# Performance work log

Measured on AMD Instinct MI355X. Metric: run time of the kernel, lower is better.

The kernel has to match this reference:

```python
import jax, jax.numpy as jnp
import numpy as np

N_NODES = 50000


def gcn_conv(x, src, dst, W, b):
    # PyG GCNConv: h = x @ W; symmetric norm with added self-loops; out = A_hat h + b
    h = x @ W
    deg = jax.ops.segment_sum(jnp.ones_like(src, dtype=h.dtype), dst,
                              num_segments=N_NODES) + 1.0  # +1 self-loop
    dis = jax.lax.rsqrt(deg)  # deg >= 1, safe
    msg = h[src] * (dis[src] * dis[dst])[:, None]          # [E,H] gather + scale
    agg = jax.ops.segment_sum(msg, dst, num_segments=N_NODES)
    agg = agg + h * (dis * dis)[:, None]                   # self-loop contribution
    return agg + b


def link_pred(zs, e, Wp, bp):
    # zs: [L,N,H]; gather endpoints along node dim, per-edge cross-layer Gram matrix
    s = zs[:, e[0]]                                # [L,E,H]
    d = zs[:, e[1]]                                # [L,E,H]
    dot = jnp.einsum('leh,meh->elm', s, d)         # [E,L,L] per-edge bmm
    emb = dot.reshape(dot.shape[0], -1)            # [E,L*L]
    return emb @ Wp + bp                           # [E,1] logits (activation=False)


def reference(x, ei, pos, neg, W0, b0, Wh, bh, Wp, bp):
    src, dst = ei[0], ei[1]
    h = jax.nn.relu(gcn_conv(x, src, dst, W0, b0))
    embs = [h]
    for i in range(Wh.shape[0]):  # fixed small layer count
        h = jax.nn.relu(gcn_conv(h, src, dst, Wh[i], bh[i]))
        embs.append(h)
    zs = jnp.stack(embs, axis=0)                   # [L,N,H]
    pos_pred = link_pred(zs, pos, Wp, bp)
    neg_pred = link_pred(zs, neg, Wp, bp)
    logits = jnp.concatenate([pos_pred, neg_pred], axis=0)  # [2E,1]
    # faithful to source: targets all zero except row index == n_pos set to 1
    targets = jnp.zeros_like(logits).at[pos_pred.shape[0]].set(1.0)
    # BCEWithLogitsLoss (mean, numerically stable)
    loss = jnp.mean(jnp.clip(logits, 0.0) - logits * targets
                    + jnp.log1p(jnp.exp(-jnp.abs(logits))))
    return loss


def setup_inputs():
    key = jax.random.key(0)
    ks = jax.random.split(key, 10)
    N, E, EP, IN, H, L = 50000, 800000, 100000, 128, 64, 4
    x = jax.random.normal(ks[0], (N, IN), jnp.float32)
    ei = jax.random.randint(ks[1], (2, E), 0, N, dtype=jnp.int32)
    pos = jax.random.randint(ks[2], (2, EP), 0, N, dtype=jnp.int32)
    neg = jax.random.randint(ks[3], (2, EP), 0, N, dtype=jnp.int32)
    def u(k, shape, fan_in):
        s = 1.0 / np.sqrt(fan_in)
        return jax.random.uniform(k, shape, jnp.float32, -s, s)
    W0 = u(ks[4], (IN, H), IN)
    b0 = u(ks[5], (H,), IN)
    Wh = u(ks[6], (L - 1, H, H), H)
    bh = u(ks[7], (L - 1, H), H)
    Wp = u(ks[8], (L * L, 1), L * L)
    bp = u(ks[9], (1,), L * L)
    return {"x": x, "ei": ei, "pos": pos, "neg": neg, "W0": W0, "b0": b0,
            "Wh": Wh, "bh": bh, "Wp": Wp, "bp": bp}
```

## Files before the change

### kernel.cpp

```cpp
#include <hip/hip_runtime.h>
#include <hip/hip_bf16.h>
#include <math.h>

constexpr int N_NODES = 50000;
constexpr int HD = 64;
constexpr int NBKT = (N_NODES + 255) / 256;

__global__ __launch_bounds__(256) void bhist_kernel(const int* __restrict__ dst,
                                                    int* __restrict__ bcnt, int E) {
    __shared__ int lh[256];
    const int t = threadIdx.x;
    lh[t] = 0;
    __syncthreads();
    const int beg = blockIdx.x * 2048;
    const int end = min(beg + 2048, E);
    for (int i = beg + t; i < end; i += 256)
        atomicAdd(&lh[dst[i] >> 8], 1);
    __syncthreads();
    if (t < NBKT && lh[t]) atomicAdd(&bcnt[t], lh[t]);
}

__global__ __launch_bounds__(256) void bscan_kernel(const int* __restrict__ bcnt,
                                                    int* __restrict__ bbase,
                                                    int* __restrict__ gcur) {
    const int t = threadIdx.x;
    const int v = (t < NBKT) ? bcnt[t] : 0;
    const int lane = t & 63, wid = t >> 6;
    int incl = v;
#pragma unroll
    for (int o = 1; o <= 32; o <<= 1) {
        int u = __shfl_up(incl, o);
        if (lane >= o) incl += u;
    }
    __shared__ int wt[4];
    if (lane == 63) wt[wid] = incl;
    __syncthreads();
    int base = 0;
    for (int w = 0; w < wid; ++w) base += wt[w];
    const int excl = base + incl - v;
    if (t < NBKT) { bbase[t] = excl; gcur[t] = excl; }
    if (t == NBKT - 1) bbase[NBKT] = excl + v;
}

__global__ __launch_bounds__(256) void partition_kernel(const int* __restrict__ src,
                                                        const int* __restrict__ dst,
                                                        int* __restrict__ gcur,
                                                        unsigned* __restrict__ pk, int E) {
    __shared__ unsigned epk[8192];
    __shared__ int lh[NBKT], lbase[NBKT], lcur[NBKT];
    const int t = threadIdx.x;
    for (int i = t; i < NBKT; i += 256) { lh[i] = 0; lcur[i] = 0; }
    __syncthreads();
    const int beg = blockIdx.x * 8192;
    const int end = min(beg + 8192, E);
    for (int i = beg + t; i < end; i += 256) {
        const int s = src[i], d = dst[i];
        const int bkt = d >> 8;
        epk[i - beg] = ((unsigned)bkt << 24) | ((unsigned)(d & 255) << 16) | (unsigned)s;
        atomicAdd(&lh[bkt], 1);
    }
    __syncthreads();
    for (int i = t; i < NBKT; i += 256)
        if (lh[i]) lbase[i] = atomicAdd(&gcur[i], lh[i]);
    __syncthreads();
    for (int i = beg + t; i < end; i += 256) {
        const unsigned p = epk[i - beg];
        const int bkt = p >> 24;
        const int r = atomicAdd(&lcur[bkt], 1);
        pk[lbase[bkt] + r] = p;
    }
}

__global__ __launch_bounds__(256) void bsort_kernel(const unsigned* __restrict__ pk,
                                                    const int* __restrict__ bbase,
                                                    int* __restrict__ off,
                                                    float* __restrict__ dis,
                                                    int* __restrict__ csr, int E, int N) {
    __shared__ int ncnt[256], nbs[256], ncur[256];
    __shared__ int wt[4];
    const int t = threadIdx.x;
    const int bkt = blockIdx.x;
    const int gb = bbase[bkt], ge = bbase[bkt + 1];
    ncnt[t] = 0; ncur[t] = 0;
    __syncthreads();
    for (int i = gb + t; i < ge; i += 256)
        atomicAdd(&ncnt[(pk[i] >> 16) & 255], 1);
    __syncthreads();
    const int v = ncnt[t];
    const int lane = t & 63, wid = t >> 6;
    int incl = v;
#pragma unroll
    for (int o = 1; o <= 32; o <<= 1) {
        int u = __shfl_up(incl, o);
        if (lane >= o) incl += u;
    }
    if (lane == 63) wt[wid] = incl;
    __syncthreads();
    int base = 0;
    for (int w = 0; w < wid; ++w) base += wt[w];
    nbs[t] = base + incl - v;
    const int n = bkt * 256 + t;
    if (n < N) {
        off[n] = gb + nbs[t];
        dis[n] = rsqrtf((float)v + 1.0f);
        if (n == N - 1) off[N] = E;
    }
    __syncthreads();
    for (int i = gb + t; i < ge; i += 256) {
        const unsigned p = pk[i];
        const int dl = (p >> 16) & 255;
        const int r = atomicAdd(&ncur[dl], 1);
        csr[gb + nbs[dl] + r] = (int)(p & 0xFFFFu);
    }
}

template <int K>
__global__ __launch_bounds__(256) void gemm_kernel(const float* __restrict__ in,
                                                   const float* __restrict__ W,
                                                   float* __restrict__ out,
                                                   unsigned short* __restrict__ out16, int N) {
    __shared__ float xs[64][68];
    __shared__ float Wl[64][64];
    const int t = threadIdx.x;
    const int row0 = blockIdx.x * 64;
    const int cq = t & 15, rq = t >> 4;
    float acc[4][4] = {{0.f}};
    for (int kc = 0; kc < K; kc += 64) {
#pragma unroll
        for (int it = 0; it < 4; ++it) {
            const int idx = it * 256 + t;
            const int r = idx >> 4, c4 = idx & 15;
            const int rr = min(row0 + r, N - 1);
            *(float4*)(&xs[r][c4 * 4]) = *(const float4*)(in + (size_t)rr * K + kc + c4 * 4);
            *(float4*)(&Wl[r][c4 * 4]) = *(const float4*)(W + (size_t)(kc + r) * HD + c4 * 4);
        }
        __syncthreads();
#pragma unroll
        for (int k4 = 0; k4 < 16; ++k4) {
            float a[4][4], b[4][4];
#pragma unroll
            for (int i = 0; i < 4; ++i)
                *(float4*)a[i] = *(const float4*)(&xs[rq * 4 + i][k4 * 4]);
#pragma unroll
            for (int kk = 0; kk < 4; ++kk)
                *(float4*)b[kk] = *(const float4*)(&Wl[k4 * 4 + kk][cq * 4]);
#pragma unroll
            for (int kk = 0; kk < 4; ++kk)
#pragma unroll
                for (int i = 0; i < 4; ++i)
#pragma unroll
                    for (int j = 0; j < 4; ++j)
                        acc[i][j] = fmaf(a[i][kk], b[kk][j], acc[i][j]);
        }
        __syncthreads();
    }
#pragma unroll
    for (int i = 0; i < 4; ++i) {
        const int r = row0 + rq * 4 + i;
        if (r < N) {
            *(float4*)(out + (size_t)r * HD + cq * 4) =
                make_float4(acc[i][0], acc[i][1], acc[i][2], acc[i][3]);
            ushort4 o16;
            __hip_bfloat16 b0 = __float2bfloat16(acc[i][0]);
            __hip_bfloat16 b1 = __float2bfloat16(acc[i][1]);
            __hip_bfloat16 b2 = __float2bfloat16(acc[i][2]);
            __hip_bfloat16 b3 = __float2bfloat16(acc[i][3]);
            o16.x = *(unsigned short*)&b0; o16.y = *(unsigned short*)&b1;
            o16.z = *(unsigned short*)&b2; o16.w = *(unsigned short*)&b3;
            *(ushort4*)(out16 + (size_t)r * HD + cq * 4) = o16;
        }
    }
}

__global__ __launch_bounds__(256) void agg_kernel(const int* __restrict__ csr,
                                                  const int* __restrict__ off,
                                                  const float* __restrict__ dis,
                                                  const float* __restrict__ hw,
                                                  const unsigned short* __restrict__ hw16,
                                                  const float* __restrict__ b,
                                                  float* __restrict__ out,
                                                  __hip_bfloat16* __restrict__ out16, int N) {
    const int lane = threadIdx.x & 63;
    const int wid  = threadIdx.x >> 6;
    const int n = blockIdx.x * 4 + wid;
    if (n >= N) return;
    const int beg = off[n];
    const int c = min(off[n + 1] - beg, 64);
    int   s_l = 0;
    float w_l = 0.f;
    if (lane < c) {
        s_l = csr[beg + lane];
        w_l = dis[s_l];
    }
    const float dn = dis[n];
    const int g = lane >> 4;
    const int p = lane & 15;
    float ax = 0.f, ay = 0.f, az = 0.f, aw = 0.f;
    for (int e = 0; e < c; e += 4) {
        const int   ee = e + g;
        const int   sE = __shfl(s_l, ee);
        const float wE = __shfl(w_l, ee);
        const ushort4 hv = *(const ushort4*)(hw16 + (size_t)sE * HD + p * 4);
        ax = fmaf(__uint_as_float((unsigned)hv.x << 16), wE, ax);
        ay = fmaf(__uint_as_float((unsigned)hv.y << 16), wE, ay);
        az = fmaf(__uint_as_float((unsigned)hv.z << 16), wE, az);
        aw = fmaf(__uint_as_float((unsigned)hv.w << 16), wE, aw);
    }
#pragma unroll
    for (int st = 16; st <= 32; st <<= 1) {
        ax += __shfl_xor(ax, st);
        ay += __shfl_xor(ay, st);
        az += __shfl_xor(az, st);
        aw += __shfl_xor(aw, st);
    }
    if (g == 0) {
        const float4 self = *(const float4*)(hw + (size_t)n * HD + p * 4);
        const float4 bv   = *(const float4*)(b + p * 4);
        float4 v;
        v.x = fmaxf(fmaf(ax + self.x * dn, dn, bv.x), 0.f);
        v.y = fmaxf(fmaf(ay + self.y * dn, dn, bv.y), 0.f);
        v.z = fmaxf(fmaf(az + self.z * dn, dn, bv.z), 0.f);
        v.w = fmaxf(fmaf(aw + self.w * dn, dn, bv.w), 0.f);
        *(float4*)(out + (size_t)n * HD + p * 4) = v;
        ushort4 o16;
        __hip_bfloat16 t0 = __float2bfloat16(v.x);
        __hip_bfloat16 t1 = __float2bfloat16(v.y);
        __hip_bfloat16 t2 = __float2bfloat16(v.z);
        __hip_bfloat16 t3 = __float2bfloat16(v.w);
        o16.x = *(unsigned short*)&t0;
        o16.y = *(unsigned short*)&t1;
        o16.z = *(unsigned short*)&t2;
        o16.w = *(unsigned short*)&t3;
        *(ushort4*)((unsigned short*)out16 + (size_t)n * HD + p * 4) = o16;
    }
}

__global__ __launch_bounds__(256) void uprep_kernel(const __hip_bfloat16* __restrict__ zs16,
                                                    const float* __restrict__ Wp,
                                                    ushort4* __restrict__ u16, int N) {
    const int i = blockIdx.x * blockDim.x + threadIdx.x;
    const int total = N * HD;
    if (i >= total) return;
    const size_t NH = (size_t)N_NODES * HD;
    float z0 = __bfloat162float(zs16[0 * NH + i]);
    float z1 = __bfloat162float(zs16[1 * NH + i]);
    float z2 = __bfloat162float(zs16[2 * NH + i]);
    float z3 = __bfloat162float(zs16[3 * NH + i]);
    ushort4 r;
    unsigned short* rp = (unsigned short*)&r;
#pragma unroll
    for (int m = 0; m < 4; ++m) {
        float um = z0 * Wp[0 * 4 + m] + z1 * Wp[1 * 4 + m] + z2 * Wp[2 * 4 + m] + z3 * Wp[3 * 4 + m];
        __hip_bfloat16 bv = __float2bfloat16(um);
        rp[m] = *(unsigned short*)&bv;
    }
    u16[i] = r;
}

__global__ __launch_bounds__(256) void linkpred_kernel(const ushort4* __restrict__ u16,
                                                       const unsigned short* __restrict__ zs16,
                                                       const int* __restrict__ pos,
                                                       const int* __restrict__ neg,
                                                       const float* __restrict__ bp,
                                                       double* __restrict__ acc, int EP) {
    const int lane = threadIdx.x & 63;
    const int wid  = threadIdx.x >> 6;
    const size_t NH = (size_t)N_NODES * HD;
    const float bpv = bp[0];
    int gw = blockIdx.x * 4 + wid;
    const int nw = gridDim.x * 4;
    const int nchunks = (2 * EP) >> 3;
    float lsum = 0.f;
    for (int c0 = gw; c0 < nchunks; c0 += nw) {
        const int c = __builtin_amdgcn_readfirstlane(c0);
        const int i0 = c << 3;
        const bool is_pos = i0 < EP;
        const int* __restrict__ eptr = is_pos ? pos : neg;
        const int jj0 = is_pos ? i0 : i0 - EP;
        float t[8];
#pragma unroll
        for (int k = 0; k < 8; ++k) {
            const int e0 = eptr[jj0 + k];
            const int e1 = eptr[EP + jj0 + k];
            ushort4 uv = u16[(size_t)e0 * HD + lane];
            const unsigned short* __restrict__ dptr = zs16 + (size_t)e1 * HD + lane;
            float u0 = __uint_as_float((unsigned)uv.x << 16);
            float u1 = __uint_as_float((unsigned)uv.y << 16);
            float u2 = __uint_as_float((unsigned)uv.z << 16);
            float u3 = __uint_as_float((unsigned)uv.w << 16);
            float d0 = __uint_as_float((unsigned)dptr[0 * NH] << 16);
            float d1 = __uint_as_float((unsigned)dptr[1 * NH] << 16);
            float d2 = __uint_as_float((unsigned)dptr[2 * NH] << 16);
            float d3 = __uint_as_float((unsigned)dptr[3 * NH] << 16);
            float s = u0 * d0;
            s = fmaf(u1, d1, s);
            s = fmaf(u2, d2, s);
            s = fmaf(u3, d3, s);
            t[k] = s;
        }
#pragma unroll
        for (int st = 1; st <= 32; st <<= 1) {
#pragma unroll
            for (int k = 0; k < 8; ++k) t[k] += __shfl_xor(t[k], st);
        }
        if (lane < 8) {
            float tt = t[0];
            tt = (lane == 1) ? t[1] : tt;
            tt = (lane == 2) ? t[2] : tt;
            tt = (lane == 3) ? t[3] : tt;
            tt = (lane == 4) ? t[4] : tt;
            tt = (lane == 5) ? t[5] : tt;
            tt = (lane == 6) ? t[6] : tt;
            tt = (lane == 7) ? t[7] : tt;
            float logit  = tt + bpv;
            float target = (i0 + lane == EP) ? 1.f : 0.f;
            lsum += fmaxf(logit, 0.f) - logit * target + log1pf(expf(-fabsf(logit)));
        }
    }
#pragma unroll
    for (int o = 32; o >= 1; o >>= 1) lsum += __shfl_xor(lsum, o);
    __shared__ float wsum[4];
    if (lane == 0) wsum[wid] = lsum;
    __syncthreads();
    if (threadIdx.x == 0) {
        double bs = (double)wsum[0] + (double)wsum[1] + (double)wsum[2] + (double)wsum[3];
        atomicAdd(acc, bs);
    }
}

__global__ void loss_final(const double* __restrict__ acc, float* __restrict__ out, int denom) {
    out[0] = (float)(acc[0] / (double)denom);
}

extern "C" void kernel_launch(void* const* d_in, const int* in_sizes, int n_in,
                              void* d_out, int out_size, void* d_ws, size_t ws_size,
                              hipStream_t stream) {
    const float* x   = (const float*)d_in[0];
    const int*   ei  = (const int*)d_in[1];
    const int*   pos = (const int*)d_in[2];
    const int*   neg = (const int*)d_in[3];
    const float* W0  = (const float*)d_in[4];
    const float* b0  = (const float*)d_in[5];
    const float* Wh  = (const float*)d_in[6];
    const float* bh  = (const float*)d_in[7];
    const float* Wp  = (const float*)d_in[8];
    const float* bp  = (const float*)d_in[9];
    const int E  = in_sizes[1] / 2;
    const int EP = in_sizes[2] / 2;
    const int N  = N_NODES;

    char* ws = (char*)d_ws;
    size_t off_b = 0;
    auto alloc = [&](size_t bytes) { char* p = ws + off_b; off_b = (off_b + bytes + 255) & ~(size_t)255; return p; };
    float* zs = (float*)alloc((size_t)4 * N * HD * sizeof(float));
    char*  hw_u = alloc((size_t)N * HD * sizeof(ushort4));
    float*   hw  = (float*)hw_u;
    ushort4* u16 = (ushort4*)hw_u;
    unsigned short* hw16 = (unsigned short*)alloc((size_t)N * HD * sizeof(unsigned short));
    __hip_bfloat16* zs16 = (__hip_bfloat16*)alloc((size_t)4 * N * HD * sizeof(__hip_bfloat16));
    float* dis = (float*)alloc((size_t)N * sizeof(float));
    int*   off = (int*)alloc((size_t)(N + 1) * sizeof(int));
    int*   csr = (int*)alloc((size_t)E * sizeof(int));
    unsigned* pk = (unsigned*)alloc((size_t)E * sizeof(unsigned));
    int*   bbase = (int*)alloc((size_t)(NBKT + 1) * sizeof(int));
    int*   gcur  = (int*)alloc((size_t)NBKT * sizeof(int));
    char*  zbase = ws + off_b;
    int*   bcnt = (int*)alloc((size_t)NBKT * sizeof(int));
    double* acc = (double*)alloc(sizeof(double));
    size_t zero_bytes = (size_t)((char*)acc - zbase) + sizeof(double);

    hipMemsetAsync(zbase, 0, zero_bytes, stream);

    const int* src = ei;
    const int* dst = ei + E;

    bhist_kernel<<<(E + 2047) / 2048, 256, 0, stream>>>(dst, bcnt, E);
    bscan_kernel<<<1, 256, 0, stream>>>(bcnt, bbase, gcur);
    partition_kernel<<<(E + 8191) / 8192, 256, 0, stream>>>(src, dst, gcur, pk, E);
    bsort_kernel<<<NBKT, 256, 0, stream>>>(pk, bbase, off, dis, csr, E, N);

    const int agg_blocks  = (N + 3) / 4;
    const int gemm_blocks = (N + 63) / 64;

    gemm_kernel<128><<<gemm_blocks, 256, 0, stream>>>(x, W0, hw, hw16, N);
    agg_kernel<<<agg_blocks, 256, 0, stream>>>(csr, off, dis, hw, hw16, b0, zs, zs16, N);

    for (int l = 1; l < 4; ++l) {
        float* zprev = zs + (size_t)(l - 1) * N * HD;
        float* zcur  = zs + (size_t)l * N * HD;
        __hip_bfloat16* zcur16 = zs16 + (size_t)l * N * HD;
        gemm_kernel<64><<<gemm_blocks, 256, 0, stream>>>(zprev, Wh + (size_t)(l - 1) * HD * HD, hw, hw16, N);
        agg_kernel<<<agg_blocks, 256, 0, stream>>>(csr, off, dis, hw, hw16,
                                                   bh + (size_t)(l - 1) * HD, zcur, zcur16, N);
    }

    uprep_kernel<<<(N * HD + 255) / 256, 256, 0, stream>>>(zs16, Wp, u16, N);
    linkpred_kernel<<<2048, 256, 0, stream>>>(u16, (const unsigned short*)zs16,
                                              pos, neg, bp, acc, EP);
    loss_final<<<1, 1, 0, stream>>>(acc, (float*)d_out, 2 * EP);
}
```

Baseline: 306.1 us.

## Store all intermediates in bf16, widen agg gathers, interleave link-pred layers

Drops the fp32 copies of hw and zs, so the GEMM reads bf16 activations and writes only bf16, and the self-loop term reads bf16. The aggregation kernel now has 8 lanes per edge, each loading 16 bytes, with a one-step software prefetch of the next row. uprep also writes a layer-interleaved d16 array so link prediction does one 8-byte load per endpoint instead of four strided 2-byte loads. Together these cut memory traffic, at the cost of more bf16 rounding in the self-loop term and the GEMM inputs, and an extra N×H×4 bf16 buffer.

```diff
diff --git a/kernel.cpp b/kernel.cpp
--- a/kernel.cpp
+++ b/kernel.cpp
@@ -5,6 +5,14 @@
 constexpr int N_NODES = 50000;
 constexpr int HD = 64;
 constexpr int NBKT = (N_NODES + 255) / 256;
+
+__device__ __forceinline__ float bf2f(unsigned short u) {
+    return __uint_as_float((unsigned)u << 16);
+}
+__device__ __forceinline__ unsigned short f2bf(float f) {
+    __hip_bfloat16 b = __float2bfloat16(f);
+    return *(unsigned short*)&b;
+}
 
 __global__ __launch_bounds__(256) void bhist_kernel(const int* __restrict__ dst,
                                                     int* __restrict__ bcnt, int E) {
@@ -114,10 +122,9 @@
     }
 }
 
-template <int K>
-__global__ __launch_bounds__(256) void gemm_kernel(const float* __restrict__ in,
+template <int K, bool INBF16>
+__global__ __launch_bounds__(256) void gemm_kernel(const void* __restrict__ in_,
                                                    const float* __restrict__ W,
-                                                   float* __restrict__ out,
                                                    unsigned short* __restrict__ out16, int N) {
     __shared__ float xs[64][68];
     __shared__ float Wl[64][64];
@@ -131,7 +138,14 @@
             const int idx = it * 256 + t;
             const int r = idx >> 4, c4 = idx & 15;
             const int rr = min(row0 + r, N - 1);
-            *(float4*)(&xs[r][c4 * 4]) = *(const float4*)(in + (size_t)rr * K + kc + c4 * 4);
+            if constexpr (INBF16) {
+                const unsigned short* in16 = (const unsigned short*)in_;
+                const ushort4 v = *(const ushort4*)(in16 + (size_t)rr * K + kc + c4 * 4);
+                *(float4*)(&xs[r][c4 * 4]) = make_float4(bf2f(v.x), bf2f(v.y), bf2f(v.z), bf2f(v.w));
+            } else {
+                const float* inf = (const float*)in_;
+                *(float4*)(&xs[r][c4 * 4]) = *(const float4*)(inf + (size_t)rr * K + kc + c4 * 4);
+            }
             *(float4*)(&Wl[r][c4 * 4]) = *(const float4*)(W + (size_t)(kc + r) * HD + c4 * 4);
         }
         __syncthreads();
@@ -158,16 +172,10 @@
     for (int i = 0; i < 4; ++i) {
         const int r = row0 + rq * 4 + i;
         if (r < N) {
-            *(float4*)(out + (size_t)r * HD + cq * 4) =
-                make_float4(acc[i][0], acc[i][1], acc[i][2], acc[i][3]);
-            ushort4 o16;
-            __hip_bfloat16 b0 = __float2bfloat16(acc[i][0]);
-            __hip_bfloat16 b1 = __float2bfloat16(acc[i][1]);
-            __hip_bfloat16 b2 = __float2bfloat16(acc[i][2]);
-            __hip_bfloat16 b3 = __float2bfloat16(acc[i][3]);
-            o16.x = *(unsigned short*)&b0; o16.y = *(unsigned short*)&b1;
-            o16.z = *(unsigned short*)&b2; o16.w = *(unsigned short*)&b3;
-            *(ushort4*)(out16 + (size_t)r * HD + cq * 4) = o16;
+            ushort4 o;
+            o.x = f2bf(acc[i][0]); o.y = f2bf(acc[i][1]);
+            o.z = f2bf(acc[i][2]); o.w = f2bf(acc[i][3]);
+            *(ushort4*)(out16 + (size_t)r * HD + cq * 4) = o;
         }
     }
 }
@@ -175,11 +183,9 @@
 __global__ __launch_bounds__(256) void agg_kernel(const int* __restrict__ csr,
                                                   const int* __restrict__ off,
                                                   const float* __restrict__ dis,
-                                                  const float* __restrict__ hw,
-                                                  const unsigned short* __restrict__ hw16,
+                                                  const unsigned short* __restrict__ h16,
                                                   const float* __restrict__ b,
-                                                  float* __restrict__ out,
-                                                  __hip_bfloat16* __restrict__ out16, int N) {
+                                                  unsigned short* __restrict__ z16, int N) {
     const int lane = threadIdx.x & 63;
     const int wid  = threadIdx.x >> 6;
     const int n = blockIdx.x * 4 + wid;
@@ -193,79 +199,91 @@
         w_l = dis[s_l];
     }
     const float dn = dis[n];
-    const int g = lane >> 4;
-    const int p = lane & 15;
-    float ax = 0.f, ay = 0.f, az = 0.f, aw = 0.f;
-    for (int e = 0; e < c; e += 4) {
-        const int   ee = e + g;
-        const int   sE = __shfl(s_l, ee);
-        const float wE = __shfl(w_l, ee);
-        const ushort4 hv = *(const ushort4*)(hw16 + (size_t)sE * HD + p * 4);
-        ax = fmaf(__uint_as_float((unsigned)hv.x << 16), wE, ax);
-        ay = fmaf(__uint_as_float((unsigned)hv.y << 16), wE, ay);
-        az = fmaf(__uint_as_float((unsigned)hv.z << 16), wE, az);
-        aw = fmaf(__uint_as_float((unsigned)hv.w << 16), wE, aw);
-    }
-#pragma unroll
-    for (int st = 16; st <= 32; st <<= 1) {
-        ax += __shfl_xor(ax, st);
-        ay += __shfl_xor(ay, st);
-        az += __shfl_xor(az, st);
-        aw += __shfl_xor(aw, st);
-    }
+    const int g = lane >> 3;
+    const int p = lane & 7;
+    float a[8];
+#pragma unroll
+    for (int j = 0; j < 8; ++j) a[j] = 0.f;
+    int   sE = __shfl(s_l, g);
+    float wE = __shfl(w_l, g);
+    uint4 hv = *(const uint4*)(h16 + (size_t)sE * HD + p * 8);
+    for (int e = 8; e < c; e += 8) {
+        const int   sN = __shfl(s_l, e + g);
+        const float wN = __shfl(w_l, e + g);
+        const uint4 nv = *(const uint4*)(h16 + (size_t)sN * HD + p * 8);
+        const unsigned vv[4] = {hv.x, hv.y, hv.z, hv.w};
+#pragma unroll
+        for (int q = 0; q < 4; ++q) {
+            a[2 * q]     = fmaf(__uint_as_float(vv[q] << 16), wE, a[2 * q]);
+            a[2 * q + 1] = fmaf(__uint_as_float(vv[q] & 0xFFFF0000u), wE, a[2 * q + 1]);
+        }
+        hv = nv; wE = wN;
+    }
+    {
+        const unsigned vv[4] = {hv.x, hv.y, hv.z, hv.w};
+#pragma unroll
+        for (int q = 0; q < 4; ++q) {
+            a[2 * q]     = fmaf(__uint_as_float(vv[q] << 16), wE, a[2 * q]);
+            a[2 * q + 1] = fmaf(__uint_as_float(vv[q] & 0xFFFF0000u), wE, a[2 * q + 1]);
+        }
+    }
+#pragma unroll
+    for (int st = 8; st <= 32; st <<= 1)
+#pragma unroll
+        for (int j = 0; j < 8; ++j) a[j] += __shfl_xor(a[j], st);
     if (g == 0) {
-        const float4 self = *(const float4*)(hw + (size_t)n * HD + p * 4);
-        const float4 bv   = *(const float4*)(b + p * 4);
-        float4 v;
-        v.x = fmaxf(fmaf(ax + self.x * dn, dn, bv.x), 0.f);
-        v.y = fmaxf(fmaf(ay + self.y * dn, dn, bv.y), 0.f);
-        v.z = fmaxf(fmaf(az + self.z * dn, dn, bv.z), 0.f);
-        v.w = fmaxf(fmaf(aw + self.w * dn, dn, bv.w), 0.f);
-        *(float4*)(out + (size_t)n * HD + p * 4) = v;
-        ushort4 o16;
-        __hip_bfloat16 t0 = __float2bfloat16(v.x);
-        __hip_bfloat16 t1 = __float2bfloat16(v.y);
-        __hip_bfloat16 t2 = __float2bfloat16(v.z);
-        __hip_bfloat16 t3 = __float2bfloat16(v.w);
-        o16.x = *(unsigned short*)&t0;
-        o16.y = *(unsigned short*)&t1;
-        o16.z = *(unsigned short*)&t2;
-        o16.w = *(unsigned short*)&t3;
-        *(ushort4*)((unsigned short*)out16 + (size_t)n * HD + p * 4) = o16;
-    }
-}
-
-__global__ __launch_bounds__(256) void uprep_kernel(const __hip_bfloat16* __restrict__ zs16,
+        const uint4 sv = *(const uint4*)(h16 + (size_t)n * HD + p * 8);
+        const unsigned ss[4] = {sv.x, sv.y, sv.z, sv.w};
+        const float4 b0 = *(const float4*)(b + p * 8);
+        const float4 b1 = *(const float4*)(b + p * 8 + 4);
+        const float bb[8] = {b0.x, b0.y, b0.z, b0.w, b1.x, b1.y, b1.z, b1.w};
+        float o[8];
+#pragma unroll
+        for (int q = 0; q < 4; ++q) {
+            o[2 * q]     = a[2 * q]     + __uint_as_float(ss[q] << 16) * dn;
+            o[2 * q + 1] = a[2 * q + 1] + __uint_as_float(ss[q] & 0xFFFF0000u) * dn;
+        }
+#pragma unroll
+        for (int j = 0; j < 8; ++j) o[j] = fmaxf(fmaf(o[j], dn, bb[j]), 0.f);
+        ushort4 o0, o1;
+        o0.x = f2bf(o[0]); o0.y = f2bf(o[1]); o0.z = f2bf(o[2]); o0.w = f2bf(o[3]);
+        o1.x = f2bf(o[4]); o1.y = f2bf(o[5]); o1.z = f2bf(o[6]); o1.w = f2bf(o[7]);
+        unsigned short* zp = z16 + (size_t)n * HD + p * 8;
+        *(ushort4*)zp = o0;
+        *(ushort4*)(zp + 4) = o1;
+    }
+}
+
+__global__ __launch_bounds__(256) void uprep_kernel(const unsigned short* __restrict__ z16,
                                                     const float* __restrict__ Wp,
-                                                    ushort4* __restrict__ u16, int N) {
+                                                    ushort4* __restrict__ u16,
+                                                    ushort4* __restrict__ d16, int N) {
     const int i = blockIdx.x * blockDim.x + threadIdx.x;
     const int total = N * HD;
     if (i >= total) return;
     const size_t NH = (size_t)N_NODES * HD;
-    float z0 = __bfloat162float(zs16[0 * NH + i]);
-    float z1 = __bfloat162float(zs16[1 * NH + i]);
-    float z2 = __bfloat162float(zs16[2 * NH + i]);
-    float z3 = __bfloat162float(zs16[3 * NH + i]);
-    ushort4 r;
-    unsigned short* rp = (unsigned short*)&r;
-#pragma unroll
-    for (int m = 0; m < 4; ++m) {
-        float um = z0 * Wp[0 * 4 + m] + z1 * Wp[1 * 4 + m] + z2 * Wp[2 * 4 + m] + z3 * Wp[3 * 4 + m];
-        __hip_bfloat16 bv = __float2bfloat16(um);
-        rp[m] = *(unsigned short*)&bv;
-    }
-    u16[i] = r;
+    const unsigned short r0 = z16[0 * NH + i], r1 = z16[1 * NH + i];
+    const unsigned short r2 = z16[2 * NH + i], r3 = z16[3 * NH + i];
+    ushort4 d;
+    d.x = r0; d.y = r1; d.z = r2; d.w = r3;
+    d16[i] = d;
+    const float z0 = bf2f(r0), z1 = bf2f(r1), z2 = bf2f(r2), z3 = bf2f(r3);
+    ushort4 u;
+    u.x = f2bf(z0 * Wp[0] + z1 * Wp[4] + z2 * Wp[8]  + z3 * Wp[12]);
+    u.y = f2bf(z0 * Wp[1] + z1 * Wp[5] + z2 * Wp[9]  + z3 * Wp[13]);
+    u.z = f2bf(z0 * Wp[2] + z1 * Wp[6] + z2 * Wp[10] + z3 * Wp[14]);
+    u.w = f2bf(z0 * Wp[3] + z1 * Wp[7] + z2 * Wp[11] + z3 * Wp[15]);
+    u16[i] = u;
 }
 
 __global__ __launch_bounds__(256) void linkpred_kernel(const ushort4* __restrict__ u16,
-                                                       const unsigned short* __restrict__ zs16,
+                                                       const ushort4* __restrict__ d16,
                                                        const int* __restrict__ pos,
                                                        const int* __restrict__ neg,
                                                        const float* __restrict__ bp,
                                                        double* __restrict__ acc, int EP) {
     const int lane = threadIdx.x & 63;
     const int wid  = threadIdx.x >> 6;
-    const size_t NH = (size_t)N_NODES * HD;
     const float bpv = bp[0];
     int gw = blockIdx.x * 4 + wid;
     const int nw = gridDim.x * 4;
@@ -282,20 +300,12 @@
         for (int k = 0; k < 8; ++k) {
             const int e0 = eptr[jj0 + k];
             const int e1 = eptr[EP + jj0 + k];
-            ushort4 uv = u16[(size_t)e0 * HD + lane];
-            const unsigned short* __restrict__ dptr = zs16 + (size_t)e1 * HD + lane;
-            float u0 = __uint_as_float((unsigned)uv.x << 16);
-            float u1 = __uint_as_float((unsigned)uv.y << 16);
-            float u2 = __uint_as_float((unsigned)uv.z << 16);
-            float u3 = __uint_as_float((unsigned)uv.w << 16);
-            float d0 = __uint_as_float((unsigned)dptr[0 * NH] << 16);
-            float d1 = __uint_as_float((unsigned)dptr[1 * NH] << 16);
-            float d2 = __uint_as_float((unsigned)dptr[2 * NH] << 16);
-            float d3 = __uint_as_float((unsigned)dptr[3 * NH] << 16);
-            float s = u0 * d0;
-            s = fmaf(u1, d1, s);
-            s = fmaf(u2, d2, s);
-            s = fmaf(u3, d3, s);
+            const ushort4 uv = u16[(size_t)e0 * HD + lane];
+            const ushort4 dv = d16[(size_t)e1 * HD + lane];
+            float s = bf2f(uv.x) * bf2f(dv.x);
+            s = fmaf(bf2f(uv.y), bf2f(dv.y), s);
+            s = fmaf(bf2f(uv.z), bf2f(dv.z), s);
+            s = fmaf(bf2f(uv.w), bf2f(dv.w), s);
             t[k] = s;
         }
 #pragma unroll
@@ -348,16 +358,15 @@
     const int E  = in_sizes[1] / 2;
     const int EP = in_sizes[2] / 2;
     const int N  = N_NODES;
+    const size_t NH = (size_t)N * HD;
 
     char* ws = (char*)d_ws;
     size_t off_b = 0;
     auto alloc = [&](size_t bytes) { char* p = ws + off_b; off_b = (off_b + bytes + 255) & ~(size_t)255; return p; };
-    float* zs = (float*)alloc((size_t)4 * N * HD * sizeof(float));
-    char*  hw_u = alloc((size_t)N * HD * sizeof(ushort4));
-    float*   hw  = (float*)hw_u;
-    ushort4* u16 = (ushort4*)hw_u;
-    unsigned short* hw16 = (unsigned short*)alloc((size_t)N * HD * sizeof(unsigned short));
-    __hip_bfloat16* zs16 = (__hip_bfloat16*)alloc((size_t)4 * N * HD * sizeof(__hip_bfloat16));
+    unsigned short* h16 = (unsigned short*)alloc(NH * sizeof(unsigned short));
+    unsigned short* z16 = (unsigned short*)alloc(4 * NH * sizeof(unsigned short));
+    ushort4* u16 = (ushort4*)alloc(NH * sizeof(ushort4));
+    ushort4* d16 = (ushort4*)alloc(NH * sizeof(ushort4));
     float* dis = (float*)alloc((size_t)N * sizeof(float));
     int*   off = (int*)alloc((size_t)(N + 1) * sizeof(int));
     int*   csr = (int*)alloc((size_t)E * sizeof(int));
@@ -382,20 +391,18 @@
     const int agg_blocks  = (N + 3) / 4;
     const int gemm_blocks = (N + 63) / 64;
 
-    gemm_kernel<128><<<gemm_blocks, 256, 0, stream>>>(x, W0, hw, hw16, N);
-    agg_kernel<<<agg_blocks, 256, 0, stream>>>(csr, off, dis, hw, hw16, b0, zs, zs16, N);
+    gemm_kernel<128, false><<<gemm_blocks, 256, 0, stream>>>(x, W0, h16, N);
+    agg_kernel<<<agg_blocks, 256, 0, stream>>>(csr, off, dis, h16, b0, z16, N);
 
     for (int l = 1; l < 4; ++l) {
-        float* zprev = zs + (size_t)(l - 1) * N * HD;
-        float* zcur  = zs + (size_t)l * N * HD;
-        __hip_bfloat16* zcur16 = zs16 + (size_t)l * N * HD;
-        gemm_kernel<64><<<gemm_blocks, 256, 0, stream>>>(zprev, Wh + (size_t)(l - 1) * HD * HD, hw, hw16, N);
-        agg_kernel<<<agg_blocks, 256, 0, stream>>>(csr, off, dis, hw, hw16,
-                                                   bh + (size_t)(l - 1) * HD, zcur, zcur16, N);
-    }
-
-    uprep_kernel<<<(N * HD + 255) / 256, 256, 0, stream>>>(zs16, Wp, u16, N);
-    linkpred_kernel<<<2048, 256, 0, stream>>>(u16, (const unsigned short*)zs16,
-                                              pos, neg, bp, acc, EP);
+        unsigned short* zprev = z16 + (size_t)(l - 1) * NH;
+        unsigned short* zcur  = z16 + (size_t)l * NH;
+        gemm_kernel<64, true><<<gemm_blocks, 256, 0, stream>>>(zprev, Wh + (size_t)(l - 1) * HD * HD, h16, N);
+        agg_kernel<<<agg_blocks, 256, 0, stream>>>(csr, off, dis, h16,
+                                                   bh + (size_t)(l - 1) * HD, zcur, N);
+    }
+
+    uprep_kernel<<<(N * HD + 255) / 256, 256, 0, stream>>>(z16, Wp, u16, d16, N);
+    linkpred_kernel<<<2048, 256, 0, stream>>>(u16, d16, pos, neg, bp, acc, EP);
     loss_final<<<1, 1, 0, stream>>>(acc, (float*)d_out, 2 * EP);
 }
```

After: 288.0 us. -5.9%, faster.
